# Performance work log

Hardware: AMD Instinct MI355X
Metric: run time of the kernel (lower is better)

## Reference

```python
import jax, jax.numpy as jnp
import numpy as np

N_NODES = 100000
N_EDGES = 1600000
IN_C, HID_C, OUT_C = 128, 128, 64


def setup_inputs() -> dict:
    key = jax.random.key(0)
    ks = jax.random.split(key, 8)
    x = jax.random.normal(ks[0], (N_NODES, IN_C), dtype=jnp.float32)
    edge_index = jax.random.randint(ks[1], (2, N_EDGES), 0, N_NODES, dtype=jnp.int64)
    # SAGEConv params: lin_l (aggregated neighbors, with bias), lin_r (root, no bias)
    s1 = 1.0 / np.sqrt(IN_C)
    s2 = 1.0 / np.sqrt(HID_C)
    W1_l = jax.random.uniform(ks[2], (IN_C, HID_C), jnp.float32, -s1, s1)
    b1_l = jnp.zeros((HID_C,), jnp.float32)
    W1_r = jax.random.uniform(ks[3], (IN_C, HID_C), jnp.float32, -s1, s1)
    W2_l = jax.random.uniform(ks[4], (HID_C, OUT_C), jnp.float32, -s2, s2)
    b2_l = jnp.zeros((OUT_C,), jnp.float32)
    W2_r = jax.random.uniform(ks[5], (HID_C, OUT_C), jnp.float32, -s2, s2)
    return {"x": x, "edge_index": edge_index, "W1_l": W1_l, "b1_l": b1_l,
            "W1_r": W1_r, "W2_l": W2_l, "b2_l": b2_l, "W2_r": W2_r}


def _sage_conv(x, src, dst, W_l, b_l, W_r):
    # gather source features, scatter-max reduce onto destinations
    msg = x[src]                                             # [E, C]
    aggr = jax.ops.segment_max(msg, dst, num_segments=N_NODES)
    aggr = jnp.where(jnp.isfinite(aggr), aggr, 0.0)          # isolated nodes -> 0 (PyG behavior)
    return aggr @ W_l + b_l + x @ W_r


def reference(x, edge_index, W1_l, b1_l, W1_r, W2_l, b2_l, W2_r):
    src, dst = edge_index[0], edge_index[1]
    h = _sage_conv(x, src, dst, W1_l, b1_l, W1_r)
    h = jax.nn.relu(h)
    # dropout is identity in eval mode
    out = _sage_conv(h, src, dst, W2_l, b2_l, W2_r)
    return out
```

## Files before the change

kernel.cpp:

```cpp
#include <hip/hip_runtime.h>
#include <cstdint>
#include <cmath>

#define NNODES 100000
#define NEDGES 1600000
#define NBKT   196
#define CAP    9216
#define BIN_CHUNK 4096
#define KP 136

typedef __attribute__((ext_vector_type(8))) __bf16 bf16x8;
typedef __attribute__((ext_vector_type(4))) float f32x4;
typedef short v2s __attribute__((ext_vector_type(2)));

__device__ __forceinline__ unsigned short f2bf_rne(float f) {
    unsigned int u = __float_as_uint(f);
    u += 0x7fffu + ((u >> 16) & 1u);
    return (unsigned short)(u >> 16);
}

__device__ __forceinline__ unsigned encdec(unsigned u) {
    return u ^ (((u & 0x80008000u) >> 15) * 0x7FFFu);
}

__device__ __forceinline__ unsigned pkmax(unsigned a, unsigned b) {
    v2s r = __builtin_elementwise_max(__builtin_bit_cast(v2s, a), __builtin_bit_cast(v2s, b));
    return __builtin_bit_cast(unsigned, r);
}

__global__ __launch_bounds__(256) void zero_kernel(int* __restrict__ p, int n) {
    int i = blockIdx.x * 256 + threadIdx.x;
    if (i < n) p[i] = 0;
}

__global__ __launch_bounds__(256) void convert_encode_kernel(const float4* __restrict__ in,
                                                             uint2* __restrict__ out, int n4) {
    int i = blockIdx.x * 256 + threadIdx.x;
    if (i >= n4) return;
    float4 v = in[i];
    uint2 o;
    o.x = encdec((unsigned)f2bf_rne(v.x) | ((unsigned)f2bf_rne(v.y) << 16));
    o.y = encdec((unsigned)f2bf_rne(v.z) | ((unsigned)f2bf_rne(v.w) << 16));
    out[i] = o;
}

__global__ __launch_bounds__(256) void convert_weights_kernel(
        const float* __restrict__ W1l, const float* __restrict__ W1r,
        const float* __restrict__ W2l, const float* __restrict__ W2r,
        unsigned short* __restrict__ T1l, unsigned short* __restrict__ T1r,
        unsigned short* __restrict__ T2l, unsigned short* __restrict__ T2r) {
    int i = blockIdx.x * 256 + threadIdx.x;
    if (i < 128 * 128) {
        int k = i >> 7, n = i & 127;
        T1l[n * KP + k] = f2bf_rne(W1l[i]);
        T1r[n * KP + k] = f2bf_rne(W1r[i]);
    }
    if (i < 128 * 64) {
        int k = i >> 6, n = i & 63;
        T2l[n * KP + k] = f2bf_rne(W2l[i]);
        T2r[n * KP + k] = f2bf_rne(W2r[i]);
    }
}

__global__ __launch_bounds__(256) void bin_kernel(
        const int* __restrict__ src, const int* __restrict__ dst,
        unsigned int* __restrict__ binArr, int* __restrict__ bucketFill, int nE) {
    __shared__ unsigned int stage[BIN_CHUNK];
    __shared__ unsigned char bof[BIN_CHUNK];
    __shared__ int cnt[256], cstart[256], cfill[256], gbase[256];
    const int tid = threadIdx.x;
    const int blockStart = blockIdx.x * BIN_CHUNK;
    const int chunkN = min(BIN_CHUNK, nE - blockStart);

    cnt[tid] = 0;
    __syncthreads();

    int myd[16], mys[16];
#pragma unroll
    for (int i = 0; i < 16; ++i) {
        int idx = i * 256 + tid;
        if (idx < chunkN) {
            myd[i] = dst[blockStart + idx];
            mys[i] = src[blockStart + idx];
            atomicAdd(&cnt[myd[i] >> 9], 1);
        }
    }
    __syncthreads();
    int v = cnt[tid];
    for (int off = 1; off < 256; off <<= 1) {
        int add = (tid >= off) ? cnt[tid - off] : 0;
        __syncthreads();
        cnt[tid] += add;
        __syncthreads();
    }
    cstart[tid] = cnt[tid] - v;
    cfill[tid] = cnt[tid] - v;
    if (tid < NBKT && v > 0) gbase[tid] = atomicAdd(&bucketFill[tid], v);
    __syncthreads();
#pragma unroll
    for (int i = 0; i < 16; ++i) {
        int idx = i * 256 + tid;
        if (idx < chunkN) {
            int b = myd[i] >> 9;
            int p = atomicAdd(&cfill[b], 1);
            stage[p] = ((unsigned)(myd[i] & 511) << 17) | (unsigned)mys[i];
            bof[p] = (unsigned char)b;
        }
    }
    __syncthreads();
#pragma unroll
    for (int i = 0; i < 16; ++i) {
        int idx = i * 256 + tid;
        if (idx < chunkN) {
            int b = bof[idx];
            int slot = gbase[b] + (idx - cstart[b]);
            if (slot < CAP) binArr[(size_t)b * CAP + slot] = stage[idx];
        }
    }
}

__global__ __launch_bounds__(512) void build_csr_kernel(
        const unsigned int* __restrict__ binArr, const int* __restrict__ bucketFill,
        unsigned int* __restrict__ sortedSrc,
        int* __restrict__ rowBeg, int* __restrict__ rowEnd) {
    __shared__ unsigned int stage[CAP];
    __shared__ int ncnt[512], nstart[512];
    const int b = blockIdx.x;
    const int t = threadIdx.x;
    const int cnt_b = min(bucketFill[b], CAP);

    ncnt[t] = 0;
    __syncthreads();
    for (int i = t; i < cnt_b; i += 512) {
        unsigned int e = binArr[(size_t)b * CAP + i];
        stage[i] = e;
        atomicAdd(&ncnt[e >> 17], 1);
    }
    __syncthreads();
    int v = ncnt[t];
    for (int off = 1; off < 512; off <<= 1) {
        int add = (t >= off) ? ncnt[t - off] : 0;
        __syncthreads();
        ncnt[t] += add;
        __syncthreads();
    }
    int start = ncnt[t] - v;
    nstart[t] = start;
    int n = (b << 9) + t;
    if (n < NNODES) {
        rowBeg[n] = b * CAP + start;
        rowEnd[n] = b * CAP + start + v;
    }
    __syncthreads();
    for (int i = t; i < cnt_b; i += 512) {
        unsigned int e = stage[i];
        int p = atomicAdd(&nstart[e >> 17], 1);
        sortedSrc[(size_t)b * CAP + p] = e & 0x1FFFFu;
    }
}

__global__ __launch_bounds__(256) void aggregate_max_pk(
        const uint4* __restrict__ xe,
        const int* __restrict__ rowBeg,
        const int* __restrict__ rowEnd,
        const unsigned int* __restrict__ sortedSrc,
        uint4* __restrict__ aggrb, int nN) {
    const int wave = threadIdx.x >> 6;
    const int lane = threadIdx.x & 63;
    const int n = blockIdx.x * 4 + wave;
    if (n >= nN) return;
    const int beg = rowBeg[n];
    const int end = rowEnd[n];
    const int grp = lane >> 4;
    const int c16 = lane & 15;

    if (end == beg) {
        if (lane < 16) {
            uint4 z; z.x = z.y = z.z = z.w = 0u;
            aggrb[(size_t)n * 16 + lane] = z;
        }
        return;
    }

    unsigned accp[4];
#pragma unroll
    for (int i = 0; i < 4; ++i) accp[i] = 0x80008000u;

    const int last = end - 1;
    for (int base = beg; base < end; base += 64) {
        int idx = base + lane;
        int myid = (int)sortedSrc[idx <= last ? idx : last];
        int m = end - base; if (m > 64) m = 64;
        for (int j = 0; j < m; j += 8) {
            int s0 = __shfl(myid, j + grp);
            int s1 = __shfl(myid, j + 4 + grp);
            uint4 p0 = xe[(size_t)s0 * 16 + c16];
            uint4 p1 = xe[(size_t)s1 * 16 + c16];
            accp[0] = pkmax(accp[0], p0.x);
            accp[1] = pkmax(accp[1], p0.y);
            accp[2] = pkmax(accp[2], p0.z);
            accp[3] = pkmax(accp[3], p0.w);
            accp[0] = pkmax(accp[0], p1.x);
            accp[1] = pkmax(accp[1], p1.y);
            accp[2] = pkmax(accp[2], p1.z);
            accp[3] = pkmax(accp[3], p1.w);
        }
    }
#pragma unroll
    for (int i = 0; i < 4; ++i) {
        unsigned v = accp[i];
        v = pkmax(v, (unsigned)__shfl_xor((int)v, 16));
        v = pkmax(v, (unsigned)__shfl_xor((int)v, 32));
        accp[i] = v;
    }
    if (lane < 16) {
        uint4 o;
        o.x = encdec(accp[0]);
        o.y = encdec(accp[1]);
        o.z = encdec(accp[2]);
        o.w = encdec(accp[3]);
        aggrb[(size_t)n * 16 + c16] = o;
    }
}

template<int BN, bool RELU, bool ENCOUT, typename OutT>
__global__ __launch_bounds__(256) void sage_gemm_mfma(
        const unsigned short* __restrict__ Aagg,
        const unsigned short* __restrict__ Aroot,
        const unsigned short* __restrict__ Wtl,
        const unsigned short* __restrict__ Wtr,
        const float* __restrict__ bias,
        OutT* __restrict__ C,
        int M) {
    constexpr int NT = BN / 16;
    __shared__ __align__(16) unsigned short Bs[BN * KP];

    const int tid = threadIdx.x;
    const int wave = tid >> 6;
    const int lane = tid & 63;
    const int quad = lane >> 4;
    const int mrow = lane & 15;

    const int rowA = blockIdx.x * 64 + wave * 16 + mrow;
    const int rowAc = (rowA < M) ? rowA : 0;
    const int rowD = blockIdx.x * 64 + wave * 16 + quad * 4;

    f32x4 acc[NT];
#pragma unroll
    for (int nt = 0; nt < NT; ++nt) acc[nt] = (f32x4){0.f, 0.f, 0.f, 0.f};

    for (int half = 0; half < 2; ++half) {
        const uint4* wsrc = (const uint4*)(half ? Wtr : Wtl);
        __syncthreads();
        for (int i = tid; i < BN * KP / 8; i += 256) ((uint4*)Bs)[i] = wsrc[i];
        __syncthreads();
#pragma unroll
        for (int kt = 0; kt < 4; ++kt) {
            bf16x8 a;
            if (half == 0) {
                a = *(const bf16x8*)(Aagg + (size_t)rowAc * 128 + kt * 32 + quad * 8);
            } else {
                uint4 t = *(const uint4*)(Aroot + (size_t)rowAc * 128 + kt * 32 + quad * 8);
                t.x = encdec(t.x); t.y = encdec(t.y); t.z = encdec(t.z); t.w = encdec(t.w);
                a = __builtin_bit_cast(bf16x8, t);
            }
#pragma unroll
            for (int nt = 0; nt < NT; ++nt) {
                bf16x8 b = *(const bf16x8*)(&Bs[(nt * 16 + mrow) * KP + kt * 32 + quad * 8]);
                acc[nt] = __builtin_amdgcn_mfma_f32_16x16x32_bf16(a, b, acc[nt], 0, 0, 0);
            }
        }
    }

#pragma unroll
    for (int nt = 0; nt < NT; ++nt) {
        int col = nt * 16 + mrow;
        float bv = bias[col];
#pragma unroll
        for (int r = 0; r < 4; ++r) {
            int grow = rowD + r;
            if (grow < M) {
                float v = acc[nt][r] + bv;
                if (RELU) v = fmaxf(v, 0.0f);
                if constexpr (ENCOUT) {
                    unsigned u = f2bf_rne(v);
                    u ^= ((u >> 15) & 1u) * 0x7FFFu;
                    C[(size_t)grow * BN + col] = (OutT)u;
                } else {
                    C[(size_t)grow * BN + col] = (OutT)v;
                }
            }
        }
    }
}

extern "C" void kernel_launch(void* const* d_in, const int* in_sizes, int n_in,
                              void* d_out, int out_size, void* d_ws, size_t ws_size,
                              hipStream_t stream) {
    const float* x   = (const float*)d_in[0];
    const int*   ei  = (const int*)d_in[1];
    const float* W1l = (const float*)d_in[2];
    const float* b1l = (const float*)d_in[3];
    const float* W1r = (const float*)d_in[4];
    const float* W2l = (const float*)d_in[5];
    const float* b2l = (const float*)d_in[6];
    const float* W2r = (const float*)d_in[7];
    float* out = (float*)d_out;

    const int* src = ei;
    const int* dst = ei + NEDGES;

    char* ws = (char*)d_ws;
    unsigned short* xe    = (unsigned short*)ws; ws += (size_t)NNODES * 128 * 2;
    unsigned short* he    = (unsigned short*)ws; ws += (size_t)NNODES * 128 * 2;
    unsigned short* aggrb = (unsigned short*)ws; ws += (size_t)NNODES * 128 * 2;
    unsigned int* binArr    = (unsigned int*)ws; ws += (size_t)NBKT * CAP * 4;
    unsigned int* sortedSrc = (unsigned int*)ws; ws += (size_t)NBKT * CAP * 4;
    int* rowBeg     = (int*)ws; ws += (size_t)NNODES * 4;
    int* rowEnd     = (int*)ws; ws += (size_t)NNODES * 4;
    int* bucketFill = (int*)ws; ws += 256 * 4;
    unsigned short* T1l = (unsigned short*)ws; ws += 128 * KP * 2;
    unsigned short* T1r = (unsigned short*)ws; ws += 128 * KP * 2;
    unsigned short* T2l = (unsigned short*)ws; ws += 64 * KP * 2;
    unsigned short* T2r = (unsigned short*)ws; ws += 64 * KP * 2;

    const int gAgg = (NNODES + 3) / 4;
    const int gGemm = (NNODES + 63) / 64;
    const int n4 = NNODES * 128 / 4;
    const int gBin = (NEDGES + BIN_CHUNK - 1) / BIN_CHUNK;

    zero_kernel<<<1, 256, 0, stream>>>(bucketFill, 256);
    convert_weights_kernel<<<64, 256, 0, stream>>>(W1l, W1r, W2l, W2r, T1l, T1r, T2l, T2r);
    convert_encode_kernel<<<(n4 + 255) / 256, 256, 0, stream>>>((const float4*)x, (uint2*)xe, n4);
    bin_kernel<<<gBin, 256, 0, stream>>>(src, dst, binArr, bucketFill, NEDGES);
    build_csr_kernel<<<NBKT, 512, 0, stream>>>(binArr, bucketFill, sortedSrc, rowBeg, rowEnd);

    aggregate_max_pk<<<gAgg, 256, 0, stream>>>((const uint4*)xe, rowBeg, rowEnd, sortedSrc,
                                               (uint4*)aggrb, NNODES);
    sage_gemm_mfma<128, true, true, unsigned short><<<gGemm, 256, 0, stream>>>(
        aggrb, xe, T1l, T1r, b1l, he, NNODES);
    aggregate_max_pk<<<gAgg, 256, 0, stream>>>((const uint4*)he, rowBeg, rowEnd, sortedSrc,
                                               (uint4*)aggrb, NNODES);
    sage_gemm_mfma<64, false, false, float><<<gGemm, 256, 0, stream>>>(
        aggrb, he, T2l, T2r, b2l, out, NNODES);
}
```

Before: 306.5 us.

## Fuse max-aggregation into MFMA GEMM and merge prep kernels

```diff
diff --git a/kernel.cpp b/kernel.cpp
--- a/kernel.cpp
+++ b/kernel.cpp
@@ -1,6 +1,5 @@
 #include <hip/hip_runtime.h>
 #include <cstdint>
-#include <cmath>
 
 #define NNODES 100000
 #define NEDGES 1600000
@@ -8,6 +7,8 @@
 #define CAP    9216
 #define BIN_CHUNK 4096
 #define KP 136
+#define GBIN ((NEDGES + BIN_CHUNK - 1) / BIN_CHUNK)
+#define GCVT (NNODES * 128 / 8 / 256)
 
 typedef __attribute__((ext_vector_type(8))) __bf16 bf16x8;
 typedef __attribute__((ext_vector_type(4))) float f32x4;
@@ -18,63 +19,55 @@
     u += 0x7fffu + ((u >> 16) & 1u);
     return (unsigned short)(u >> 16);
 }
-
 __device__ __forceinline__ unsigned encdec(unsigned u) {
     return u ^ (((u & 0x80008000u) >> 15) * 0x7FFFu);
 }
-
 __device__ __forceinline__ unsigned pkmax(unsigned a, unsigned b) {
     v2s r = __builtin_elementwise_max(__builtin_bit_cast(v2s, a), __builtin_bit_cast(v2s, b));
     return __builtin_bit_cast(unsigned, r);
 }
 
-__global__ __launch_bounds__(256) void zero_kernel(int* __restrict__ p, int n) {
-    int i = blockIdx.x * 256 + threadIdx.x;
-    if (i < n) p[i] = 0;
-}
-
-__global__ __launch_bounds__(256) void convert_encode_kernel(const float4* __restrict__ in,
-                                                             uint2* __restrict__ out, int n4) {
-    int i = blockIdx.x * 256 + threadIdx.x;
-    if (i >= n4) return;
-    float4 v = in[i];
-    uint2 o;
-    o.x = encdec((unsigned)f2bf_rne(v.x) | ((unsigned)f2bf_rne(v.y) << 16));
-    o.y = encdec((unsigned)f2bf_rne(v.z) | ((unsigned)f2bf_rne(v.w) << 16));
-    out[i] = o;
-}
-
-__global__ __launch_bounds__(256) void convert_weights_kernel(
+__global__ __launch_bounds__(256) void prep1_kernel(
         const float* __restrict__ W1l, const float* __restrict__ W1r,
         const float* __restrict__ W2l, const float* __restrict__ W2r,
         unsigned short* __restrict__ T1l, unsigned short* __restrict__ T1r,
-        unsigned short* __restrict__ T2l, unsigned short* __restrict__ T2r) {
+        unsigned short* __restrict__ T2l, unsigned short* __restrict__ T2r,
+        int* __restrict__ bucketFill) {
+    if (blockIdx.x == 64) { bucketFill[threadIdx.x] = 0; return; }
     int i = blockIdx.x * 256 + threadIdx.x;
-    if (i < 128 * 128) {
-        int k = i >> 7, n = i & 127;
-        T1l[n * KP + k] = f2bf_rne(W1l[i]);
-        T1r[n * KP + k] = f2bf_rne(W1r[i]);
-    }
+    int k = i >> 7, n = i & 127;
+    T1l[n * KP + k] = f2bf_rne(W1l[i]);
+    T1r[n * KP + k] = f2bf_rne(W1r[i]);
     if (i < 128 * 64) {
-        int k = i >> 6, n = i & 63;
-        T2l[n * KP + k] = f2bf_rne(W2l[i]);
-        T2r[n * KP + k] = f2bf_rne(W2r[i]);
-    }
-}
-
-__global__ __launch_bounds__(256) void bin_kernel(
+        int k2 = i >> 6, n2 = i & 63;
+        T2l[n2 * KP + k2] = f2bf_rne(W2l[i]);
+        T2r[n2 * KP + k2] = f2bf_rne(W2r[i]);
+    }
+}
+
+__global__ __launch_bounds__(256) void prep2_kernel(
         const int* __restrict__ src, const int* __restrict__ dst,
-        unsigned int* __restrict__ binArr, int* __restrict__ bucketFill, int nE) {
+        unsigned int* __restrict__ binArr, int* __restrict__ bucketFill,
+        const float4* __restrict__ xin, uint4* __restrict__ xeout, int nE) {
+    if (blockIdx.x >= GBIN) {
+        int i = (blockIdx.x - GBIN) * 256 + threadIdx.x;
+        float4 v0 = xin[(size_t)2 * i], v1 = xin[(size_t)2 * i + 1];
+        uint4 o;
+        o.x = encdec((unsigned)f2bf_rne(v0.x) | ((unsigned)f2bf_rne(v0.y) << 16));
+        o.y = encdec((unsigned)f2bf_rne(v0.z) | ((unsigned)f2bf_rne(v0.w) << 16));
+        o.z = encdec((unsigned)f2bf_rne(v1.x) | ((unsigned)f2bf_rne(v1.y) << 16));
+        o.w = encdec((unsigned)f2bf_rne(v1.z) | ((unsigned)f2bf_rne(v1.w) << 16));
+        xeout[i] = o;
+        return;
+    }
     __shared__ unsigned int stage[BIN_CHUNK];
     __shared__ unsigned char bof[BIN_CHUNK];
     __shared__ int cnt[256], cstart[256], cfill[256], gbase[256];
     const int tid = threadIdx.x;
     const int blockStart = blockIdx.x * BIN_CHUNK;
     const int chunkN = min(BIN_CHUNK, nE - blockStart);
-
     cnt[tid] = 0;
     __syncthreads();
-
     int myd[16], mys[16];
 #pragma unroll
     for (int i = 0; i < 16; ++i) {
@@ -128,7 +121,6 @@
     const int b = blockIdx.x;
     const int t = threadIdx.x;
     const int cnt_b = min(bucketFill[b], CAP);
-
     ncnt[t] = 0;
     __syncthreads();
     for (int i = t; i < cnt_b; i += 512) {
@@ -159,119 +151,146 @@
     }
 }
 
-__global__ __launch_bounds__(256) void aggregate_max_pk(
-        const uint4* __restrict__ xe,
+template<int BN, bool RELU, bool ENCOUT, typename OutT>
+__global__ __launch_bounds__(256, 4) void sage_fused(
+        const uint4* __restrict__ xe4,
         const int* __restrict__ rowBeg,
         const int* __restrict__ rowEnd,
         const unsigned int* __restrict__ sortedSrc,
-        uint4* __restrict__ aggrb, int nN) {
-    const int wave = threadIdx.x >> 6;
-    const int lane = threadIdx.x & 63;
-    const int n = blockIdx.x * 4 + wave;
-    if (n >= nN) return;
-    const int beg = rowBeg[n];
-    const int end = rowEnd[n];
-    const int grp = lane >> 4;
-    const int c16 = lane & 15;
-
-    if (end == beg) {
-        if (lane < 16) {
-            uint4 z; z.x = z.y = z.z = z.w = 0u;
-            aggrb[(size_t)n * 16 + lane] = z;
-        }
-        return;
-    }
-
-    unsigned accp[4];
-#pragma unroll
-    for (int i = 0; i < 4; ++i) accp[i] = 0x80008000u;
-
-    const int last = end - 1;
-    for (int base = beg; base < end; base += 64) {
-        int idx = base + lane;
-        int myid = (int)sortedSrc[idx <= last ? idx : last];
-        int m = end - base; if (m > 64) m = 64;
-        for (int j = 0; j < m; j += 8) {
-            int s0 = __shfl(myid, j + grp);
-            int s1 = __shfl(myid, j + 4 + grp);
-            uint4 p0 = xe[(size_t)s0 * 16 + c16];
-            uint4 p1 = xe[(size_t)s1 * 16 + c16];
-            accp[0] = pkmax(accp[0], p0.x);
-            accp[1] = pkmax(accp[1], p0.y);
-            accp[2] = pkmax(accp[2], p0.z);
-            accp[3] = pkmax(accp[3], p0.w);
-            accp[0] = pkmax(accp[0], p1.x);
-            accp[1] = pkmax(accp[1], p1.y);
-            accp[2] = pkmax(accp[2], p1.z);
-            accp[3] = pkmax(accp[3], p1.w);
-        }
-    }
-#pragma unroll
-    for (int i = 0; i < 4; ++i) {
-        unsigned v = accp[i];
-        v = pkmax(v, (unsigned)__shfl_xor((int)v, 16));
-        v = pkmax(v, (unsigned)__shfl_xor((int)v, 32));
-        accp[i] = v;
-    }
-    if (lane < 16) {
-        uint4 o;
-        o.x = encdec(accp[0]);
-        o.y = encdec(accp[1]);
-        o.z = encdec(accp[2]);
-        o.w = encdec(accp[3]);
-        aggrb[(size_t)n * 16 + c16] = o;
-    }
-}
-
-template<int BN, bool RELU, bool ENCOUT, typename OutT>
-__global__ __launch_bounds__(256) void sage_gemm_mfma(
-        const unsigned short* __restrict__ Aagg,
-        const unsigned short* __restrict__ Aroot,
         const unsigned short* __restrict__ Wtl,
         const unsigned short* __restrict__ Wtr,
         const float* __restrict__ bias,
         OutT* __restrict__ C,
         int M) {
     constexpr int NT = BN / 16;
-    __shared__ __align__(16) unsigned short Bs[BN * KP];
+    __shared__ __align__(16) unsigned short As[64 * KP];
+    __shared__ __align__(16) unsigned short Bs[BN * 68];
 
     const int tid = threadIdx.x;
-    const int wave = tid >> 6;
+    const int w = tid >> 6;
     const int lane = tid & 63;
+    const int grp = lane >> 4;
+    const int c16 = lane & 15;
+    const int mrow = lane & 15;
     const int quad = lane >> 4;
-    const int mrow = lane & 15;
-
-    const int rowA = blockIdx.x * 64 + wave * 16 + mrow;
-    const int rowAc = (rowA < M) ? rowA : 0;
-    const int rowD = blockIdx.x * 64 + wave * 16 + quad * 4;
+    const int base0 = blockIdx.x * 64;
+
+    int bl = 0, el = 0;
+    {
+        int nn = base0 + w * 16 + (lane & 15);
+        if (nn < M) { bl = rowBeg[nn]; el = rowEnd[nn]; }
+    }
+    int nbeg = __shfl(bl, 0), nend = __shfl(el, 0);
+    int nid = (nend > nbeg) ? (int)sortedSrc[min(nbeg + lane, nend - 1)] : 0;
+    for (int i = 0; i < 16; ++i) {
+        const int beg = nbeg, end = nend;
+        const int myid = nid;
+        if (i < 15) {
+            nbeg = __shfl(bl, i + 1);
+            nend = __shfl(el, i + 1);
+            nid = (nend > nbeg) ? (int)sortedSrc[min(nbeg + lane, nend - 1)] : 0;
+        }
+        const int r = w * 16 + i;
+        if (end <= beg) {
+            if (lane < 16) {
+                uint4 z; z.x = z.y = z.z = z.w = 0u;
+                ((uint4*)As)[r * 17 + c16] = z;
+            }
+            continue;
+        }
+        unsigned a0 = 0x80008000u, a1 = 0x80008000u, a2 = 0x80008000u, a3 = 0x80008000u;
+        {
+            const int m = min(end - beg, 64);
+            for (int j = 0; j < m; j += 16) {
+                int s0 = __shfl(myid, j + grp);
+                int s1 = __shfl(myid, j + 4 + grp);
+                int s2 = __shfl(myid, j + 8 + grp);
+                int s3 = __shfl(myid, j + 12 + grp);
+                uint4 p0 = xe4[(size_t)s0 * 16 + c16];
+                uint4 p1 = xe4[(size_t)s1 * 16 + c16];
+                uint4 p2 = xe4[(size_t)s2 * 16 + c16];
+                uint4 p3 = xe4[(size_t)s3 * 16 + c16];
+                a0 = pkmax(a0, pkmax(pkmax(p0.x, p1.x), pkmax(p2.x, p3.x)));
+                a1 = pkmax(a1, pkmax(pkmax(p0.y, p1.y), pkmax(p2.y, p3.y)));
+                a2 = pkmax(a2, pkmax(pkmax(p0.z, p1.z), pkmax(p2.z, p3.z)));
+                a3 = pkmax(a3, pkmax(pkmax(p0.w, p1.w), pkmax(p2.w, p3.w)));
+            }
+        }
+        for (int bs = beg + 64; bs < end; bs += 64) {
+            int bid = (int)sortedSrc[min(bs + lane, end - 1)];
+            const int m = min(end - bs, 64);
+            for (int j = 0; j < m; j += 16) {
+                int s0 = __shfl(bid, j + grp);
+                int s1 = __shfl(bid, j + 4 + grp);
+                int s2 = __shfl(bid, j + 8 + grp);
+                int s3 = __shfl(bid, j + 12 + grp);
+                uint4 p0 = xe4[(size_t)s0 * 16 + c16];
+                uint4 p1 = xe4[(size_t)s1 * 16 + c16];
+                uint4 p2 = xe4[(size_t)s2 * 16 + c16];
+                uint4 p3 = xe4[(size_t)s3 * 16 + c16];
+                a0 = pkmax(a0, pkmax(pkmax(p0.x, p1.x), pkmax(p2.x, p3.x)));
+                a1 = pkmax(a1, pkmax(pkmax(p0.y, p1.y), pkmax(p2.y, p3.y)));
+                a2 = pkmax(a2, pkmax(pkmax(p0.z, p1.z), pkmax(p2.z, p3.z)));
+                a3 = pkmax(a3, pkmax(pkmax(p0.w, p1.w), pkmax(p2.w, p3.w)));
+            }
+        }
+        a0 = pkmax(a0, (unsigned)__shfl_xor((int)a0, 16));
+        a1 = pkmax(a1, (unsigned)__shfl_xor((int)a1, 16));
+        a2 = pkmax(a2, (unsigned)__shfl_xor((int)a2, 16));
+        a3 = pkmax(a3, (unsigned)__shfl_xor((int)a3, 16));
+        a0 = pkmax(a0, (unsigned)__shfl_xor((int)a0, 32));
+        a1 = pkmax(a1, (unsigned)__shfl_xor((int)a1, 32));
+        a2 = pkmax(a2, (unsigned)__shfl_xor((int)a2, 32));
+        a3 = pkmax(a3, (unsigned)__shfl_xor((int)a3, 32));
+        if (lane < 16) {
+            uint4 o;
+            o.x = encdec(a0); o.y = encdec(a1); o.z = encdec(a2); o.w = encdec(a3);
+            ((uint4*)As)[r * 17 + c16] = o;
+        }
+    }
 
     f32x4 acc[NT];
 #pragma unroll
     for (int nt = 0; nt < NT; ++nt) acc[nt] = (f32x4){0.f, 0.f, 0.f, 0.f};
+    __syncthreads();
 
     for (int half = 0; half < 2; ++half) {
-        const uint4* wsrc = (const uint4*)(half ? Wtr : Wtl);
-        __syncthreads();
-        for (int i = tid; i < BN * KP / 8; i += 256) ((uint4*)Bs)[i] = wsrc[i];
-        __syncthreads();
-#pragma unroll
-        for (int kt = 0; kt < 4; ++kt) {
-            bf16x8 a;
-            if (half == 0) {
-                a = *(const bf16x8*)(Aagg + (size_t)rowAc * 128 + kt * 32 + quad * 8);
-            } else {
-                uint4 t = *(const uint4*)(Aroot + (size_t)rowAc * 128 + kt * 32 + quad * 8);
-                t.x = encdec(t.x); t.y = encdec(t.y); t.z = encdec(t.z); t.w = encdec(t.w);
-                a = __builtin_bit_cast(bf16x8, t);
-            }
-#pragma unroll
-            for (int nt = 0; nt < NT; ++nt) {
-                bf16x8 b = *(const bf16x8*)(&Bs[(nt * 16 + mrow) * KP + kt * 32 + quad * 8]);
-                acc[nt] = __builtin_amdgcn_mfma_f32_16x16x32_bf16(a, b, acc[nt], 0, 0, 0);
-            }
-        }
-    }
-
+        if (half == 1) {
+            __syncthreads();
+            const uint2* xs = (const uint2*)xe4;
+            for (int i2 = tid; i2 < 64 * 32; i2 += 256) {
+                int r = i2 >> 5, c = i2 & 31;
+                int gr = base0 + r;
+                if (gr >= M) gr = 0;
+                uint2 vv = xs[(size_t)gr * 32 + c];
+                vv.x = encdec(vv.x); vv.y = encdec(vv.y);
+                ((uint2*)As)[r * 34 + c] = vv;
+            }
+        }
+        const unsigned short* Wt = half ? Wtr : Wtl;
+        for (int ks = 0; ks < 2; ++ks) {
+            __syncthreads();
+            const uint2* wsrc = (const uint2*)Wt;
+            for (int i2 = tid; i2 < BN * 16; i2 += 256) {
+                int n = i2 >> 4, c = i2 & 15;
+                ((uint2*)Bs)[n * 17 + c] = wsrc[n * 34 + ks * 16 + c];
+            }
+            __syncthreads();
+#pragma unroll
+            for (int kt2 = 0; kt2 < 2; ++kt2) {
+                bf16x8 a = *(const bf16x8*)(As + (w * 16 + mrow) * KP +
+                                            ks * 64 + kt2 * 32 + quad * 8);
+#pragma unroll
+                for (int nt = 0; nt < NT; ++nt) {
+                    bf16x8 b = *(const bf16x8*)(Bs + (nt * 16 + mrow) * 68 +
+                                                kt2 * 32 + quad * 8);
+                    acc[nt] = __builtin_amdgcn_mfma_f32_16x16x32_bf16(a, b, acc[nt], 0, 0, 0);
+                }
+            }
+        }
+    }
+
+    const int rowD = base0 + w * 16 + quad * 4;
 #pragma unroll
     for (int nt = 0; nt < NT; ++nt) {
         int col = nt * 16 + mrow;
@@ -311,9 +330,8 @@
     const int* dst = ei + NEDGES;
 
     char* ws = (char*)d_ws;
-    unsigned short* xe    = (unsigned short*)ws; ws += (size_t)NNODES * 128 * 2;
-    unsigned short* he    = (unsigned short*)ws; ws += (size_t)NNODES * 128 * 2;
-    unsigned short* aggrb = (unsigned short*)ws; ws += (size_t)NNODES * 128 * 2;
+    unsigned short* xe = (unsigned short*)ws; ws += (size_t)NNODES * 128 * 2;
+    unsigned short* he = (unsigned short*)ws; ws += (size_t)NNODES * 128 * 2;
     unsigned int* binArr    = (unsigned int*)ws; ws += (size_t)NBKT * CAP * 4;
     unsigned int* sortedSrc = (unsigned int*)ws; ws += (size_t)NBKT * CAP * 4;
     int* rowBeg     = (int*)ws; ws += (size_t)NNODES * 4;
@@ -324,23 +342,15 @@
     unsigned short* T2l = (unsigned short*)ws; ws += 64 * KP * 2;
     unsigned short* T2r = (unsigned short*)ws; ws += 64 * KP * 2;
 
-    const int gAgg = (NNODES + 3) / 4;
     const int gGemm = (NNODES + 63) / 64;
-    const int n4 = NNODES * 128 / 4;
-    const int gBin = (NEDGES + BIN_CHUNK - 1) / BIN_CHUNK;
-
-    zero_kernel<<<1, 256, 0, stream>>>(bucketFill, 256);
-    convert_weights_kernel<<<64, 256, 0, stream>>>(W1l, W1r, W2l, W2r, T1l, T1r, T2l, T2r);
-    convert_encode_kernel<<<(n4 + 255) / 256, 256, 0, stream>>>((const float4*)x, (uint2*)xe, n4);
-    bin_kernel<<<gBin, 256, 0, stream>>>(src, dst, binArr, bucketFill, NEDGES);
+
+    prep1_kernel<<<65, 256, 0, stream>>>(W1l, W1r, W2l, W2r, T1l, T1r, T2l, T2r, bucketFill);
+    prep2_kernel<<<GBIN + GCVT, 256, 0, stream>>>(src, dst, binArr, bucketFill,
+                                                  (const float4*)x, (uint4*)xe, NEDGES);
     build_csr_kernel<<<NBKT, 512, 0, stream>>>(binArr, bucketFill, sortedSrc, rowBeg, rowEnd);
 
-    aggregate_max_pk<<<gAgg, 256, 0, stream>>>((const uint4*)xe, rowBeg, rowEnd, sortedSrc,
-                                               (uint4*)aggrb, NNODES);
-    sage_gemm_mfma<128, true, true, unsigned short><<<gGemm, 256, 0, stream>>>(
-        aggrb, xe, T1l, T1r, b1l, he, NNODES);
-    aggregate_max_pk<<<gAgg, 256, 0, stream>>>((const uint4*)he, rowBeg, rowEnd, sortedSrc,
-                                               (uint4*)aggrb, NNODES);
-    sage_gemm_mfma<64, false, false, float><<<gGemm, 256, 0, stream>>>(
-        aggrb, he, T2l, T2r, b2l, out, NNODES);
-}
+    sage_fused<128, true, true, unsigned short><<<gGemm, 256, 0, stream>>>(
+        (const uint4*)xe, rowBeg, rowEnd, sortedSrc, T1l, T1r, b1l, he, NNODES);
+    sage_fused<64, false, false, float><<<gGemm, 256, 0, stream>>>(
+        (const uint4*)he, rowBeg, rowEnd, sortedSrc, T2l, T2r, b2l, out, NNODES);
+}
```

Result: no change. 304.2 us (-0.8%).
